# Kernel tuning notes

Measured on AMD Instinct MI355X. Metric: run time of the kernel, lower is better.

Reference implementation:

```python
import jax, jax.numpy as jnp
import numpy as np

N_SUBJECTS = 16
N_LABELS = 8
DENS_TEMP = 0.1  # args.ProtoSim_dens_temp


def setup_inputs() -> dict:
    key = jax.random.key(0)
    k1, k2, k3 = jax.random.split(key, 3)
    B, C, D = 16384, 2, 1024
    X_data = jax.random.normal(k1, (B, C, D), dtype=jnp.float32)
    subject = jax.random.randint(k2, (B,), 0, N_SUBJECTS, dtype=jnp.int64) if jax.config.jax_enable_x64 else jax.random.randint(k2, (B,), 0, N_SUBJECTS).astype(jnp.int32)
    labels = jax.random.randint(k3, (B,), 0, N_LABELS).astype(subject.dtype)
    return {"X_data": X_data, "subject": subject, "labels": labels}


def reference(X_data, subject, labels):
    B, C, D = X_data.shape
    K = N_SUBJECTS * N_LABELS  # all (subject,label) groups assumed present
    # contrast_feature = cat(unbind(X_data, 1), 0) -> [B*C, D]
    feat = X_data.swapaxes(0, 1).reshape(B * C, D)
    sub2 = jnp.tile(subject, C)          # cat((subject, subject))
    lab2 = jnp.tile(labels, C)
    # torch.unique sorts -> group g = subject * N_LABELS + label matches loop order
    gid = sub2 * N_LABELS + lab2
    counts = jax.ops.segment_sum(jnp.ones((B * C,), feat.dtype), gid, num_segments=K)  # (K,)
    centroid = jax.ops.segment_sum(feat, gid, num_segments=K) / counts[:, None]       # (K, D)
    # per-row euclidean distance to own group centroid (torch.cdist to 1 point)
    dist = jnp.linalg.norm(feat - centroid[gid], axis=1)                               # (B*C,)
    mean_sqrt = jax.ops.segment_sum(jnp.sqrt(dist), gid, num_segments=K) / counts
    density = mean_sqrt / jnp.log(counts + 10.0)
    density = jnp.where(counts <= 1.0, density.max(), density)
    density = jnp.clip(density, jnp.quantile(density, 0.1), jnp.quantile(density, 0.9))
    density = DENS_TEMP * density / density.mean()                                     # (K,)
    # masks: positives = same label, different subject
    g_sub = jnp.arange(K) // N_LABELS
    g_lab = jnp.arange(K) % N_LABELS
    subj_mask = (sub2[:, None] != g_sub[None, :]).astype(feat.dtype)  # (B*C, K)
    lab_mask = (lab2[:, None] == g_lab[None, :]).astype(feat.dtype)
    mask = subj_mask * lab_mask
    # every row has N_SUBJECTS-1 positives (all groups present), so no row filtering
    sim = (feat @ centroid.T) / density[None, :]                                        # (B*C, K)
    sim = sim - sim.max(axis=1, keepdims=True)
    pos = sim * mask
    logp = jax.nn.log_softmax(pos, axis=1)
    row_loss = -(mask * logp).sum(axis=1) / mask.sum(axis=1)  # soft-target CE / #pos
    return row_loss.reshape(C, B).mean()
```

## Files before the change

### kernel.cpp

```cpp
#include <hip/hip_runtime.h>
#include <hip/hip_bf16.h>
#include <math.h>

#define NSUB 16
#define NLAB 8
#define KG 128
#define BN 16384
#define DD 1024

typedef float v4f __attribute__((ext_vector_type(4)));
typedef short short8v __attribute__((ext_vector_type(8)));
typedef unsigned short ushort4v __attribute__((ext_vector_type(4)));

static __device__ __forceinline__ short f2bf(float f) {
    unsigned u = __builtin_bit_cast(unsigned, f);
    unsigned r = (u + 0x7fffu + ((u >> 16) & 1u)) >> 16;
    return (short)r;
}

static __device__ __forceinline__ float bf2f(unsigned short u) {
    unsigned v = ((unsigned)u) << 16;
    return __builtin_bit_cast(float, v);
}

static __device__ __forceinline__ unsigned packbf2(float x, float y) {
    union { __hip_bfloat162 h; unsigned u; } c;
    c.h = __float22bfloat162_rn(float2{x, y});
    return c.u;
}

__global__ __launch_bounds__(1024) void k0_gid(const int* __restrict__ subject,
                                               const int* __restrict__ labels,
                                               int* __restrict__ gid, int* __restrict__ hist) {
    __shared__ int h[KG];
    int t = threadIdx.x;
    if (t < KG) h[t] = 0;
    __syncthreads();
    int b = blockIdx.x * 1024 + t;
    int g = subject[b] * NLAB + labels[b];
    gid[b] = g;
    atomicAdd(&h[g], 1);
    __syncthreads();
    if (t < KG) hist[blockIdx.x * KG + t] = h[t];
}

__global__ __launch_bounds__(1024) void k0c_scatter(const int* __restrict__ gid,
                                                    const int* __restrict__ hist,
                                                    int* __restrict__ cnt,
                                                    int* __restrict__ rowlist) {
    __shared__ int tots[KG], base0[KG], lcur[KG];
    int t = threadIdx.x, bi = blockIdx.x;
    if (t < KG) {
        int tot = 0, pre = 0;
#pragma unroll
        for (int j = 0; j < 16; ++j) {
            int v = hist[j * KG + t];
            tot += v;
            if (j < bi) pre += v;
        }
        tots[t] = tot;
        base0[t] = pre;
        lcur[t] = 0;
        if (bi == 0) cnt[t] = tot;
    }
    __syncthreads();
    if (t < KG) {
        int o = 0;
        for (int j = 0; j < t; ++j) o += tots[j];
        base0[t] += o;
    }
    __syncthreads();
    int b = bi * 1024 + t;
    int g = gid[b];
    rowlist[base0[g] + atomicAdd(&lcur[g], 1)] = b;
}

__global__ __launch_bounds__(256) void k1_centroid(const float* __restrict__ X,
                                                   const int* __restrict__ rowlist,
                                                   const int* __restrict__ cnt,
                                                   unsigned short* __restrict__ Btil,
                                                   float* __restrict__ cnormPart) {
    int g = blockIdx.x >> 1;
    int half = blockIdx.x & 1;
    int t = threadIdx.x, lane = t & 63, w = t >> 6;
    int c = t >> 7, td = t & 127;
    __shared__ int rows[512];
    __shared__ int sh_no[2];
    __shared__ float acc4[256][4];
    __shared__ float wsum[2];
    if (w == 0) {
        int v = 0;
        if (lane < g) v += cnt[lane];
        if (lane + 64 < g) v += cnt[lane + 64];
#pragma unroll
        for (int x = 32; x; x >>= 1) v += __shfl_xor(v, x, 64);
        if (lane == 0) { sh_no[0] = v; sh_no[1] = cnt[g]; }
    }
    __syncthreads();
    int o = sh_no[0], n = min(sh_no[1], 512);
    for (int i = t; i < n; i += 256) rows[i] = rowlist[o + i];
    __syncthreads();
    size_t coff = (size_t)c * 1024 + half * 512 + td * 4;
    float4 s4 = make_float4(0.f, 0.f, 0.f, 0.f);
    int i = 0;
    for (; i + 8 <= n; i += 8) {
        float4 v[8];
#pragma unroll
        for (int u = 0; u < 8; ++u)
            v[u] = *(const float4*)(X + (size_t)rows[i + u] * 2048 + coff);
#pragma unroll
        for (int u = 0; u < 8; ++u) {
            s4.x += v[u].x; s4.y += v[u].y; s4.z += v[u].z; s4.w += v[u].w;
        }
    }
    for (; i < n; ++i) {
        float4 v = *(const float4*)(X + (size_t)rows[i] * 2048 + coff);
        s4.x += v.x; s4.y += v.y; s4.z += v.z; s4.w += v.w;
    }
    acc4[t][0] = s4.x; acc4[t][1] = s4.y; acc4[t][2] = s4.z; acc4[t][3] = s4.w;
    __syncthreads();
    float s = 0.f;
    if (t < 128) {
        float inv = 1.f / (2.f * (float)n);
        float cx[4];
#pragma unroll
        for (int j = 0; j < 4; ++j) {
            cx[j] = (acc4[t][j] + acc4[t + 128][j]) * inv;
            s += cx[j] * cx[j];
        }
        int dd = half * 512 + t * 4;
        int base_t = (dd >> 5) * 512 + ((dd >> 3) & 3) * 128 + (g & 15) * 8 + (dd & 7);
        uint2 st;
        st.x = packbf2(cx[0], cx[1]);
        st.y = packbf2(cx[2], cx[3]);
        *(uint2*)(Btil + (size_t)(g >> 4) * 16384 + base_t) = st;
    }
#pragma unroll
    for (int x = 32; x; x >>= 1) s += __shfl_xor(s, x, 64);
    if (lane == 0) wsum[w & 1] = (w < 2) ? s : 0.f;
    __syncthreads();
    if (t == 0) cnormPart[half * KG + g] = wsum[0] + wsum[1];
}

__global__ __launch_bounds__(256) void k2_tile(const float* __restrict__ X,
                                               unsigned short* __restrict__ Atil) {
    __shared__ unsigned lds[8192];
    int t = threadIdx.x, lane = t & 63, w = t >> 6;
    int rt = blockIdx.x;
#pragma unroll
    for (int p = 0; p < 4; ++p) {
        int m = w * 4 + p;
        int r = rt * 16 + m;
        const float* xp = X + (size_t)(r & (BN - 1)) * 2048 + (size_t)(r >> 14) * 1024;
        unsigned swz = (unsigned)((m & 7) << 2);
        unsigned mbase = (unsigned)m * 512;
#pragma unroll
        for (int j = 0; j < 4; ++j) {
            int d0 = j * 256 + lane * 4;
            float4 v = *(const float4*)(xp + d0);
            unsigned wi = mbase + (((unsigned)(d0 >> 1)) ^ swz);
            lds[wi] = packbf2(v.x, v.y);
            lds[wi + 1] = packbf2(v.z, v.w);
        }
    }
    __syncthreads();
    size_t gbase = (size_t)rt * 16384;
#pragma unroll
    for (int p = 0; p < 8; ++p) {
        int wo = p * 1024 + t * 4;
        int kc = wo >> 8;
        int q = (wo >> 6) & 3;
        int m = (wo >> 2) & 15;
        unsigned wi = (unsigned)m * 512 +
                      (((unsigned)(kc * 16 + q * 4)) ^ (unsigned)((m & 7) << 2));
        uint4 val = *(const uint4*)&lds[wi];
        *(uint4*)(Atil + gbase + (size_t)wo * 2) = val;
    }
}

__global__ __launch_bounds__(256) void k5a_dot(const unsigned short* __restrict__ Atil,
                                               const unsigned short* __restrict__ Btil,
                                               const int* __restrict__ gid,
                                               const float* __restrict__ cnormPart,
                                               unsigned short* __restrict__ Dotb,
                                               float* __restrict__ sqsPart) {
    __shared__ float h[KG];
    __shared__ float cnormS[KG];
    int t = threadIdx.x, lane = t & 63, w = t >> 6;
    if (t < KG) {
        h[t] = 0.f;
        cnormS[t] = cnormPart[t] + cnormPart[KG + t];
    }
    __syncthreads();
    int rt = blockIdx.x * 4 + w;
    int m = lane & 15, q = lane >> 4;
    const unsigned short* ap = Atil + (size_t)rt * 16384 + lane * 8;
    const unsigned short* bp = Btil + lane * 8;

    v4f acc[8];
#pragma unroll
    for (int j = 0; j < 8; ++j) acc[j] = (v4f){0.f, 0.f, 0.f, 0.f};

    short8v Af[2], Bf[2][8];
#pragma unroll
    for (int p = 0; p < 2; ++p) {
        Af[p] = *(const short8v*)(ap + p * 512);
#pragma unroll
        for (int gt = 0; gt < 8; ++gt)
            Bf[p][gt] = *(const short8v*)(bp + (size_t)gt * 16384 + p * 512);
    }
    float s0 = 0.f;
#pragma unroll
    for (int kc = 0; kc < 32; ++kc) {
        const int cur = kc & 1;
        short8v nA, nB[8];
        if (kc + 2 < 32) {
            nA = *(const short8v*)(ap + (kc + 2) * 512);
#pragma unroll
            for (int gt = 0; gt < 8; ++gt)
                nB[gt] = *(const short8v*)(bp + (size_t)gt * 16384 + (kc + 2) * 512);
        }
#pragma unroll
        for (int gt = 0; gt < 8; ++gt)
            acc[gt] = __builtin_amdgcn_mfma_f32_16x16x32_bf16(Af[cur], Bf[cur][gt], acc[gt], 0, 0, 0);
        {
            union { short8v s; unsigned u[4]; } ua;
            ua.s = Af[cur];
#pragma unroll
            for (int r = 0; r < 4; ++r) {
                float l0 = __builtin_bit_cast(float, ua.u[r] << 16);
                float h0 = __builtin_bit_cast(float, ua.u[r] & 0xffff0000u);
                s0 = fmaf(l0, l0, s0); s0 = fmaf(h0, h0, s0);
            }
        }
        if (kc + 2 < 32) {
            Af[cur] = nA;
#pragma unroll
            for (int gt = 0; gt < 8; ++gt) Bf[cur][gt] = nB[gt];
        }
    }

    s0 += __shfl_xor(s0, 16, 64); s0 += __shfl_xor(s0, 32, 64);

    int bid = blockIdx.x;
#pragma unroll
    for (int reg = 0; reg < 4; ++reg) {
        int rr = w * 16 + q * 4 + reg;
        int row = bid * 64 + rr;
        int b = row & (BN - 1);
        int g = gid[b];
        float own = 0.f;
#pragma unroll
        for (int gt = 0; gt < 8; ++gt) {
            float v = acc[gt][reg];
            size_t idx = (((size_t)bid * 32 + gt * 4 + (m >> 2)) * 64 + rr) * 4 + (m & 3);
            Dotb[idx] = (unsigned short)f2bf(v);
            if ((g >> 4) == gt) own = v;
        }
        float rn = __shfl(s0, q * 4 + reg, 64);
        if ((g & 15) == m) {
            float d2 = fmaxf(rn - 2.f * own + cnormS[g], 0.f);
            atomicAdd(&h[g], sqrtf(sqrtf(d2)));
        }
    }
    __syncthreads();
    if (t < KG) sqsPart[(size_t)blockIdx.x * KG + t] = h[t];
}

__global__ __launch_bounds__(128) void k5b_loss(const unsigned short* __restrict__ Dotb,
                                                const int* __restrict__ gid,
                                                const float* __restrict__ sqsPart,
                                                const int* __restrict__ cnt,
                                                float* __restrict__ out) {
    __shared__ float tmp[KG], d1s[KG], qv[4];
    __shared__ float recipDen[KG];
    __shared__ float wsum[2];
    int t = threadIdx.x;
    float cntf = 0.f, d0v = 0.f, v = 0.f;
    if (t < KG) {
        float ss = 0.f;
        for (int j = 0; j < 512; j += 4)
            ss += sqsPart[(size_t)j * KG + t] + sqsPart[(size_t)(j + 1) * KG + t] +
                  sqsPart[(size_t)(j + 2) * KG + t] + sqsPart[(size_t)(j + 3) * KG + t];
        cntf = 2.f * (float)cnt[t];
        d0v = (ss / cntf) / logf(cntf + 10.f);
        tmp[t] = d0v;
    }
    __syncthreads();
    if (t < KG) {
        float dmax = -INFINITY;
        for (int j = 0; j < KG; ++j) dmax = fmaxf(dmax, tmp[j]);
        v = (cntf <= 1.f) ? dmax : d0v;
        d1s[t] = v;
    }
    __syncthreads();
    if (t < KG) {
        int less = 0, eq = 0;
        for (int j = 0; j < KG; ++j) {
            float u = d1s[j];
            less += (u < v) ? 1 : 0;
            eq += (u == v) ? 1 : 0;
        }
        const int ppos[4] = {12, 13, 114, 115};
        for (int qq = 0; qq < 4; ++qq)
            if (less <= ppos[qq] && ppos[qq] < less + eq) qv[qq] = v;
    }
    __syncthreads();
    if (t < KG) {
        float q10 = 0.3f * qv[0] + 0.7f * qv[1];
        float q90 = 0.7f * qv[2] + 0.3f * qv[3];
        tmp[t] = fminf(fmaxf(v, q10), q90);
    }
    __syncthreads();
    if (t < KG) {
        float sum = 0.f;
        for (int j = 0; j < KG; ++j) sum += tmp[j];
        float mean = sum / (float)KG;
        recipDen[t] = mean / (0.1f * tmp[t]);
    }
    __syncthreads();
    int row = blockIdx.x * 128 + t;
    int b = row & (BN - 1);
    int g = gid[b];
    int s = g >> 3, l = g & 7;
    int lane = t & 63, w = t >> 6;
    size_t rowblk = (size_t)(row >> 6);
    const ushort4v* dp = (const ushort4v*)Dotb;
    float mx = -INFINITY;
    float psave[16];
#pragma unroll
    for (int c = 0; c < 16; ++c) {
        size_t i0 = (rowblk * 32 + c * 2) * 64 + lane;
        ushort4v dv0 = dp[i0];
        ushort4v dv1 = dp[i0 + 64];
        const float* rv = &recipDen[c * 8];
        float x[8];
#pragma unroll
        for (int j = 0; j < 4; ++j) x[j] = bf2f((unsigned short)dv0[j]) * rv[j];
#pragma unroll
        for (int j = 0; j < 4; ++j) x[4 + j] = bf2f((unsigned short)dv1[j]) * rv[4 + j];
#pragma unroll
        for (int j = 0; j < 8; ++j) mx = fmaxf(mx, x[j]);
        float sel = x[0];
#pragma unroll
        for (int j = 1; j < 8; ++j) sel = (j == l) ? x[j] : sel;
        psave[c] = sel;
    }
    float S = 0.f, P = 0.f;
#pragma unroll
    for (int j = 0; j < 16; ++j) {
        float pv = psave[j] - mx;
        float e = expf(pv);
        bool use = (j != s);
        S += use ? e : 0.f;
        P += use ? pv : 0.f;
    }
    float ll = logf(113.f + S) - P * (1.f / 15.f);
#pragma unroll
    for (int x2 = 32; x2; x2 >>= 1) ll += __shfl_xor(ll, x2, 64);
    if (lane == 0) wsum[w] = ll;
    __syncthreads();
    if (t == 0) atomicAdd(out, (wsum[0] + wsum[1]) * (1.f / 32768.f));
}

extern "C" void kernel_launch(void* const* d_in, const int* in_sizes, int n_in,
                              void* d_out, int out_size, void* d_ws, size_t ws_size,
                              hipStream_t stream) {
    const float* X = (const float*)d_in[0];
    const int* subject = (const int*)d_in[1];
    const int* labels = (const int*)d_in[2];
    float* out = (float*)d_out;
    char* w = (char*)d_ws;
    int* gid = (int*)(w + 0);
    int* hist = (int*)(w + 65536);
    int* cnt = (int*)(w + 73728);
    float* cnormPart = (float*)(w + 74240);
    int* rowlist = (int*)(w + 131072);
    float* sqsPart = (float*)(w + 262144);
    unsigned short* Btil = (unsigned short*)(w + 524288);
    unsigned short* Atil = (unsigned short*)(w + 2097152);
    unsigned short* Dotb = (unsigned short*)(w + 100663296);

    (void)hipMemsetAsync(out, 0, sizeof(float), stream);

    k2_tile<<<2048, 256, 0, stream>>>(X, Atil);
    k0_gid<<<16, 1024, 0, stream>>>(subject, labels, gid, hist);
    k0c_scatter<<<16, 1024, 0, stream>>>(gid, hist, cnt, rowlist);
    k1_centroid<<<KG * 2, 256, 0, stream>>>(X, rowlist, cnt, Btil, cnormPart);
    k5a_dot<<<512, 256, 0, stream>>>(Atil, Btil, gid, cnormPart, Dotb, sqsPart);
    k5b_loss<<<256, 128, 0, stream>>>(Dotb, gid, sqsPart, cnt, out);
}
```

Before: 266.1 us.

## Replace scatter-gather centroid build with chunked LDS-atomic partial sums and reduction

Removes the row-list scatter kernel and the gather-based centroid kernel. A new kernel streams X in row chunks and accumulates per-group column sums in shared memory with atomics, writing per-chunk partials. A second kernel reduces those partials, derives group counts from the histogram, and emits the bf16 tiled centroids and centroid norms. X is now read in a streaming order instead of through random row gathers, at the cost of shared-memory atomic contention and an extra 16MB partial buffer written and read back.

```diff
diff --git a/kernel.cpp b/kernel.cpp
--- a/kernel.cpp
+++ b/kernel.cpp
@@ -44,102 +44,78 @@
     if (t < KG) hist[blockIdx.x * KG + t] = h[t];
 }
 
-__global__ __launch_bounds__(1024) void k0c_scatter(const int* __restrict__ gid,
-                                                    const int* __restrict__ hist,
-                                                    int* __restrict__ cnt,
-                                                    int* __restrict__ rowlist) {
-    __shared__ int tots[KG], base0[KG], lcur[KG];
-    int t = threadIdx.x, bi = blockIdx.x;
-    if (t < KG) {
-        int tot = 0, pre = 0;
-#pragma unroll
-        for (int j = 0; j < 16; ++j) {
-            int v = hist[j * KG + t];
-            tot += v;
-            if (j < bi) pre += v;
-        }
-        tots[t] = tot;
-        base0[t] = pre;
-        lcur[t] = 0;
-        if (bi == 0) cnt[t] = tot;
-    }
-    __syncthreads();
-    if (t < KG) {
-        int o = 0;
-        for (int j = 0; j < t; ++j) o += tots[j];
-        base0[t] += o;
-    }
-    __syncthreads();
-    int b = bi * 1024 + t;
-    int g = gid[b];
-    rowlist[base0[g] + atomicAdd(&lcur[g], 1)] = b;
-}
-
-__global__ __launch_bounds__(256) void k1_centroid(const float* __restrict__ X,
-                                                   const int* __restrict__ rowlist,
-                                                   const int* __restrict__ cnt,
-                                                   unsigned short* __restrict__ Btil,
-                                                   float* __restrict__ cnormPart) {
-    int g = blockIdx.x >> 1;
-    int half = blockIdx.x & 1;
-    int t = threadIdx.x, lane = t & 63, w = t >> 6;
-    int c = t >> 7, td = t & 127;
-    __shared__ int rows[512];
-    __shared__ int sh_no[2];
-    __shared__ float acc4[256][4];
-    __shared__ float wsum[2];
-    if (w == 0) {
-        int v = 0;
-        if (lane < g) v += cnt[lane];
-        if (lane + 64 < g) v += cnt[lane + 64];
-#pragma unroll
-        for (int x = 32; x; x >>= 1) v += __shfl_xor(v, x, 64);
-        if (lane == 0) { sh_no[0] = v; sh_no[1] = cnt[g]; }
-    }
-    __syncthreads();
-    int o = sh_no[0], n = min(sh_no[1], 512);
-    for (int i = t; i < n; i += 256) rows[i] = rowlist[o + i];
-    __syncthreads();
-    size_t coff = (size_t)c * 1024 + half * 512 + td * 4;
+__global__ __launch_bounds__(256) void k1n_part(const float* __restrict__ X,
+                                                const int* __restrict__ gid,
+                                                float* __restrict__ part) {
+    __shared__ float acc[KG * 64];
+    __shared__ int rg[1024];
+    int t = threadIdx.x, lane = t & 63, sw = t >> 6;
+    int rc = blockIdx.x >> 4, dc = blockIdx.x & 15;
+    for (int i = t; i < KG * 64; i += 256) acc[i] = 0.f;
+    int rbase = rc * 1024;
+    for (int i = t; i < 1024; i += 256) rg[i] = gid[(rbase + i) >> 1];
+    __syncthreads();
+    const float* xp = X + (size_t)rbase * 1024 + dc * 64 + lane;
+    for (int i = sw * 8; i < 1024; i += 32) {
+        float v[8]; int g8[8];
+#pragma unroll
+        for (int u = 0; u < 8; ++u) {
+            v[u] = xp[(size_t)(i + u) * 1024];
+            g8[u] = rg[i + u];
+        }
+#pragma unroll
+        for (int u = 0; u < 8; ++u)
+            atomicAdd(&acc[g8[u] * 64 + lane], v[u]);
+    }
+    __syncthreads();
+    for (int idx = t; idx < KG * 64; idx += 256) {
+        int g = idx >> 6, dl = idx & 63;
+        part[((size_t)rc * KG + g) * 1024 + dc * 64 + dl] = acc[idx];
+    }
+}
+
+__global__ __launch_bounds__(256) void k1r_reduce(const float* __restrict__ part,
+                                                  const int* __restrict__ hist,
+                                                  unsigned short* __restrict__ Btil,
+                                                  float* __restrict__ cnormPart,
+                                                  int* __restrict__ cnt) {
+    int g = blockIdx.x, t = threadIdx.x, lane = t & 63, w = t >> 6;
+    __shared__ int scnt[16];
+    __shared__ float wsum[4];
+    __shared__ int n_sh;
+    if (t < 16) scnt[t] = hist[t * KG + g];
+    __syncthreads();
+    if (t == 0) {
+        int n = 0;
+        for (int j = 0; j < 16; ++j) n += scnt[j];
+        cnt[g] = n;
+        n_sh = n;
+    }
+    __syncthreads();
     float4 s4 = make_float4(0.f, 0.f, 0.f, 0.f);
-    int i = 0;
-    for (; i + 8 <= n; i += 8) {
-        float4 v[8];
-#pragma unroll
-        for (int u = 0; u < 8; ++u)
-            v[u] = *(const float4*)(X + (size_t)rows[i + u] * 2048 + coff);
-#pragma unroll
-        for (int u = 0; u < 8; ++u) {
-            s4.x += v[u].x; s4.y += v[u].y; s4.z += v[u].z; s4.w += v[u].w;
-        }
-    }
-    for (; i < n; ++i) {
-        float4 v = *(const float4*)(X + (size_t)rows[i] * 2048 + coff);
+    const float* pp = part + (size_t)g * 1024 + t * 4;
+#pragma unroll
+    for (int rc = 0; rc < 32; ++rc) {
+        float4 v = *(const float4*)(pp + (size_t)rc * KG * 1024);
         s4.x += v.x; s4.y += v.y; s4.z += v.z; s4.w += v.w;
     }
-    acc4[t][0] = s4.x; acc4[t][1] = s4.y; acc4[t][2] = s4.z; acc4[t][3] = s4.w;
-    __syncthreads();
-    float s = 0.f;
-    if (t < 128) {
-        float inv = 1.f / (2.f * (float)n);
-        float cx[4];
-#pragma unroll
-        for (int j = 0; j < 4; ++j) {
-            cx[j] = (acc4[t][j] + acc4[t + 128][j]) * inv;
-            s += cx[j] * cx[j];
-        }
-        int dd = half * 512 + t * 4;
-        int base_t = (dd >> 5) * 512 + ((dd >> 3) & 3) * 128 + (g & 15) * 8 + (dd & 7);
-        uint2 st;
-        st.x = packbf2(cx[0], cx[1]);
-        st.y = packbf2(cx[2], cx[3]);
-        *(uint2*)(Btil + (size_t)(g >> 4) * 16384 + base_t) = st;
-    }
+    float inv = 1.f / (2.f * (float)n_sh);
+    float cx[4] = {s4.x * inv, s4.y * inv, s4.z * inv, s4.w * inv};
+    int d0 = t * 4;
+    int base_t = (d0 >> 5) * 512 + ((d0 >> 3) & 3) * 128 + (g & 15) * 8 + (d0 & 7);
+    uint2 st;
+    st.x = packbf2(cx[0], cx[1]);
+    st.y = packbf2(cx[2], cx[3]);
+    *(uint2*)(Btil + (size_t)(g >> 4) * 16384 + base_t) = st;
+    float s = cx[0] * cx[0] + cx[1] * cx[1] + cx[2] * cx[2] + cx[3] * cx[3];
 #pragma unroll
     for (int x = 32; x; x >>= 1) s += __shfl_xor(s, x, 64);
-    if (lane == 0) wsum[w & 1] = (w < 2) ? s : 0.f;
-    __syncthreads();
-    if (t == 0) cnormPart[half * KG + g] = wsum[0] + wsum[1];
+    if (lane == 0) wsum[w] = s;
+    __syncthreads();
+    if (t == 0) {
+        cnormPart[g] = wsum[0] + wsum[1] + wsum[2] + wsum[3];
+        cnormPart[KG + g] = 0.f;
+    }
 }
 
 __global__ __launch_bounds__(256) void k2_tile(const float* __restrict__ X,
@@ -375,18 +351,18 @@
     int* hist = (int*)(w + 65536);
     int* cnt = (int*)(w + 73728);
     float* cnormPart = (float*)(w + 74240);
-    int* rowlist = (int*)(w + 131072);
     float* sqsPart = (float*)(w + 262144);
     unsigned short* Btil = (unsigned short*)(w + 524288);
     unsigned short* Atil = (unsigned short*)(w + 2097152);
+    float* part = (float*)(w + 71303168);
     unsigned short* Dotb = (unsigned short*)(w + 100663296);
 
     (void)hipMemsetAsync(out, 0, sizeof(float), stream);
 
     k2_tile<<<2048, 256, 0, stream>>>(X, Atil);
     k0_gid<<<16, 1024, 0, stream>>>(subject, labels, gid, hist);
-    k0c_scatter<<<16, 1024, 0, stream>>>(gid, hist, cnt, rowlist);
-    k1_centroid<<<KG * 2, 256, 0, stream>>>(X, rowlist, cnt, Btil, cnormPart);
+    k1n_part<<<512, 256, 0, stream>>>(X, gid, part);
+    k1r_reduce<<<KG, 256, 0, stream>>>(part, hist, Btil, cnormPart, cnt);
     k5a_dot<<<512, 256, 0, stream>>>(Atil, Btil, gid, cnormPart, Dotb, sqsPart);
     k5b_loss<<<256, 128, 0, stream>>>(Dotb, gid, sqsPart, cnt, out);
 }
```

After: 415.4 us. 1.56x slower.
